# Kernel tuning notes

Hardware: AMD Instinct MI355X
Metric: run time of the kernel (lower is better)

## Reference

```python
import jax, jax.numpy as jnp
import numpy as np
from jax import lax

D_MODEL = 1024
EXPAND = 2
D_INNER = EXPAND * D_MODEL        # 2048
D_STATE = 16
D_CONV = 4
DT_RANK = (D_MODEL + 15) // 16    # 64, standard 'auto' dt_rank
BATCH, SEQ = 2, 1024


def setup_inputs() -> dict:
    key = jax.random.key(0)
    ks = jax.random.split(key, 10)
    g = lambda k, shape, sc: jax.random.normal(k, shape, jnp.float32) * sc
    A_log = jnp.log(jnp.broadcast_to(
        jnp.arange(1, D_STATE + 1, dtype=jnp.float32), (D_INNER, D_STATE)))
    return {
        "x": jax.random.normal(ks[0], (BATCH, SEQ, D_MODEL), jnp.float32),
        "gamma": jnp.ones((D_MODEL,), jnp.float32),
        "beta": jnp.zeros((D_MODEL,), jnp.float32),
        "W_in": g(ks[1], (D_MODEL, 2 * D_INNER), 0.02),
        "W_conv": g(ks[2], (D_INNER, D_CONV), 0.1),
        "b_conv": jnp.zeros((D_INNER,), jnp.float32),
        "W_x": g(ks[3], (D_INNER, DT_RANK + 2 * D_STATE), 0.02),
        "W_dt": g(ks[4], (DT_RANK, D_INNER), 0.1),
        "b_dt": g(ks[5], (D_INNER,), 0.1),
        "A_log": A_log,
        "Dskip": jnp.ones((D_INNER,), jnp.float32),
        "W_out": g(ks[6], (D_INNER, D_MODEL), 0.02),
    }


def _layernorm(x, gamma, beta, eps=1e-5):
    mu = jnp.mean(x, axis=-1, keepdims=True)
    var = jnp.mean(jnp.square(x - mu), axis=-1, keepdims=True)
    return (x - mu) * lax.rsqrt(var + eps) * gamma + beta


def _mamba_block(x, gamma, beta, W_in, W_conv, b_conv, W_x, W_dt, b_dt,
                 A_log, Dskip, W_out):
    h = _layernorm(x, gamma, beta)                       # [B,L,D]
    xz = h @ W_in                                        # [B,L,2*Din]
    xi, z = jnp.split(xz, 2, axis=-1)                    # each [B,L,Din]

    # depthwise causal conv over time
    xt = xi.transpose(0, 2, 1)                           # [B,Din,L]
    conv = lax.conv_general_dilated(
        xt, W_conv[:, None, :], window_strides=(1,),
        padding=[(D_CONV - 1, 0)], feature_group_count=D_INNER)
    u = jax.nn.silu(conv + b_conv[None, :, None]).transpose(0, 2, 1)  # [B,L,Din]

    x_dbl = u @ W_x                                      # [B,L,dt_rank+2N]
    dt_r = x_dbl[..., :DT_RANK]
    Bm = x_dbl[..., DT_RANK:DT_RANK + D_STATE]           # [B,L,N]
    Cm = x_dbl[..., DT_RANK + D_STATE:]                  # [B,L,N]
    dt = jax.nn.softplus(dt_r @ W_dt + b_dt)             # [B,L,Din]

    A = -jnp.exp(A_log)                                  # [Din,N]

    def step(hstate, inp):
        dt_s, B_s, C_s, u_s = inp                        # [B,Din],[B,N],[B,N],[B,Din]
        dA = jnp.exp(dt_s[..., None] * A)                # [B,Din,N]
        hstate = dA * hstate + (dt_s * u_s)[..., None] * B_s[:, None, :]
        y = jnp.einsum('bdn,bn->bd', hstate, C_s)
        return hstate, y

    h0 = jnp.zeros((x.shape[0], D_INNER, D_STATE), x.dtype)
    _, ys = lax.scan(step, h0, (dt.transpose(1, 0, 2), Bm.transpose(1, 0, 2),
                                Cm.transpose(1, 0, 2), u.transpose(1, 0, 2)))
    y = ys.transpose(1, 0, 2) + u * Dskip                # [B,L,Din]
    y = y * jax.nn.silu(z)
    return x + y @ W_out                                 # residual


def reference(x, gamma, beta, W_in, W_conv, b_conv, W_x, W_dt, b_dt,
              A_log, Dskip, W_out):
    return _mamba_block(x, gamma, beta, W_in, W_conv, b_conv, W_x, W_dt,
                        b_dt, A_log, Dskip, W_out)
```

## Files before the change

### kernel.cpp

```cpp
#include <hip/hip_runtime.h>
#include <math.h>

#define BB 2
#define SS 1024
#define DM 1024
#define DI 2048
#define DSTATE 16
#define DTR 64
#define NX 96
#define ROWS (BB*SS)
#define NCHUNK 16
#define LC (SS/NCHUNK)
#define NCH (BB*DI)
#define TS 16
#define NT (LC/TS)
#define KSPLIT 4
#define KSX 16

typedef __bf16 bf16x8 __attribute__((ext_vector_type(8)));
typedef float f32x4 __attribute__((ext_vector_type(4)));

static __device__ __forceinline__ unsigned short f2bf(float f) {
    unsigned u = __builtin_bit_cast(unsigned, f);
    unsigned r = (u + 0x7fff + ((u >> 16) & 1)) >> 16;
    return (unsigned short)r;
}
static __device__ __forceinline__ float bf2f(unsigned short v) {
    return __builtin_bit_cast(float, ((unsigned)v) << 16);
}

__device__ __forceinline__ void transpose_body(const float* __restrict__ W,
                                               unsigned short* __restrict__ WT,
                                               int K, int N, int bx, int by,
                                               unsigned short (*tile)[33]) {
    int n0 = bx * 32, k0 = by * 32;
    int tx = threadIdx.x & 31, ty = threadIdx.x >> 5;
#pragma unroll
    for (int r = 0; r < 4; r++)
        tile[ty + r * 8][tx] = f2bf(W[(size_t)(k0 + ty + r * 8) * N + n0 + tx]);
    __syncthreads();
#pragma unroll
    for (int r = 0; r < 4; r++)
        WT[(size_t)(n0 + ty + r * 8) * K + k0 + tx] = tile[tx][ty + r * 8];
}

__global__ __launch_bounds__(256) void prep_kernel(const float* __restrict__ x,
                                                   const float* __restrict__ gamma,
                                                   const float* __restrict__ beta,
                                                   unsigned short* __restrict__ h,
                                                   const float* __restrict__ W_in,
                                                   unsigned short* __restrict__ W_inT,
                                                   const float* __restrict__ W_out,
                                                   unsigned short* __restrict__ W_outT,
                                                   const float* __restrict__ W_x,
                                                   unsigned short* __restrict__ W_xT,
                                                   const float* __restrict__ W_dt,
                                                   unsigned short* __restrict__ W_dtT) {
    __shared__ unsigned short tile[32][33];
    __shared__ float red[4], red2[4];
    int blk = blockIdx.x;
    if (blk < ROWS) {
        int row = blk;
        const float* xr = x + (size_t)row * DM;
        float v[4];
        float s = 0.f;
#pragma unroll
        for (int i = 0; i < 4; i++) { v[i] = xr[threadIdx.x + i * 256]; s += v[i]; }
        int lane = threadIdx.x & 63, wid = threadIdx.x >> 6;
#pragma unroll
        for (int m = 1; m < 64; m <<= 1) s += __shfl_xor(s, m);
        if (lane == 0) red[wid] = s;
        __syncthreads();
        float mean = (red[0] + red[1] + red[2] + red[3]) * (1.0f / DM);
        float vs = 0.f;
#pragma unroll
        for (int i = 0; i < 4; i++) { float dv = v[i] - mean; vs += dv * dv; }
#pragma unroll
        for (int m = 1; m < 64; m <<= 1) vs += __shfl_xor(vs, m);
        if (lane == 0) red2[wid] = vs;
        __syncthreads();
        float var = (red2[0] + red2[1] + red2[2] + red2[3]) * (1.0f / DM);
        float inv = rsqrtf(var + 1e-5f);
        unsigned short* hr = h + (size_t)row * DM;
#pragma unroll
        for (int i = 0; i < 4; i++) {
            int idx = threadIdx.x + i * 256;
            hr[idx] = f2bf((v[i] - mean) * inv * gamma[idx] + beta[idx]);
        }
        return;
    }
    blk -= ROWS;
    if (blk < 4096) { transpose_body(W_in, W_inT, DM, 2 * DI, blk % 128, blk / 128, tile); return; }
    blk -= 4096;
    if (blk < 2048) { transpose_body(W_out, W_outT, DI, DM, blk % 32, blk / 32, tile); return; }
    blk -= 2048;
    if (blk < 192) { transpose_body(W_x, W_xT, DI, NX, blk % 3, blk / 3, tile); return; }
    blk -= 192;
    transpose_body(W_dt, W_dtT, DTR, DI, blk % 64, blk / 64, tile);
}

__global__ __launch_bounds__(256) void gemm_mfma_bfout(const __bf16* __restrict__ A,
                                                       const __bf16* __restrict__ BT,
                                                       unsigned short* __restrict__ C,
                                                       int M, int N, int K) {
    __shared__ __bf16 As[128 * 32];
    __shared__ __bf16 Bs[128 * 32];
    int tid = threadIdx.x;
    int w = tid >> 6, lane = tid & 63;
    int wr = w >> 1, wc = w & 1;
    int m0 = blockIdx.y * 128, n0 = blockIdx.x * 128;
    f32x4 acc[4][4] = {};
    int srow = lane >> 2, sgran = lane & 3;
    const __bf16* gA = A + (size_t)(m0 + w * 32) * K;
    const __bf16* gB = BT + (size_t)(n0 + w * 32) * K;
    int fr = lane & 15, q = lane >> 4;

    for (int k0 = 0; k0 < K; k0 += 32) {
        __syncthreads();
#pragma unroll
        for (int c = 0; c < 2; c++) {
            const __bf16* ga = gA + (size_t)(c * 16 + srow) * K + k0 + sgran * 8;
            const __bf16* gb = gB + (size_t)(c * 16 + srow) * K + k0 + sgran * 8;
            __builtin_amdgcn_global_load_lds(
                (const __attribute__((address_space(1))) void*)ga,
                (__attribute__((address_space(3))) void*)&As[(w * 32 + c * 16) * 32], 16, 0, 0);
            __builtin_amdgcn_global_load_lds(
                (const __attribute__((address_space(1))) void*)gb,
                (__attribute__((address_space(3))) void*)&Bs[(w * 32 + c * 16) * 32], 16, 0, 0);
        }
        __syncthreads();
        bf16x8 af[4], bfr[4];
#pragma unroll
        for (int i = 0; i < 4; i++)
            af[i] = *(const bf16x8*)&As[(wr * 64 + i * 16 + fr) * 32 + q * 8];
#pragma unroll
        for (int j = 0; j < 4; j++)
            bfr[j] = *(const bf16x8*)&Bs[(wc * 64 + j * 16 + fr) * 32 + q * 8];
#pragma unroll
        for (int i = 0; i < 4; i++)
#pragma unroll
            for (int j = 0; j < 4; j++)
                acc[i][j] = __builtin_amdgcn_mfma_f32_16x16x32_bf16(af[i], bfr[j], acc[i][j], 0, 0, 0);
    }
#pragma unroll
    for (int i = 0; i < 4; i++)
#pragma unroll
        for (int j = 0; j < 4; j++)
#pragma unroll
            for (int r = 0; r < 4; r++) {
                size_t ro = (size_t)(m0 + wr * 64 + i * 16 + q * 4 + r) * N
                          + n0 + wc * 64 + j * 16 + fr;
                C[ro] = f2bf(acc[i][j][r]);
            }
}

__global__ __launch_bounds__(256) void gemm_mfma_splitk(const __bf16* __restrict__ A,
                                                        const __bf16* __restrict__ BT,
                                                        unsigned short* __restrict__ part,
                                                        int M, int N, int K) {
    __shared__ __bf16 As[128 * 32];
    __shared__ __bf16 Bs[128 * 32];
    int tid = threadIdx.x;
    int w = tid >> 6, lane = tid & 63;
    int wr = w >> 1, wc = w & 1;
    int m0 = blockIdx.y * 128, n0 = blockIdx.x * 128;
    int ks = K / KSPLIT;
    int kbase = blockIdx.z * ks;
    f32x4 acc[4][4] = {};
    int srow = lane >> 2, sgran = lane & 3;
    const __bf16* gA = A + (size_t)(m0 + w * 32) * K + kbase;
    const __bf16* gB = BT + (size_t)(n0 + w * 32) * K + kbase;
    int fr = lane & 15, q = lane >> 4;

    for (int k0 = 0; k0 < ks; k0 += 32) {
        __syncthreads();
#pragma unroll
        for (int c = 0; c < 2; c++) {
            const __bf16* ga = gA + (size_t)(c * 16 + srow) * K + k0 + sgran * 8;
            const __bf16* gb = gB + (size_t)(c * 16 + srow) * K + k0 + sgran * 8;
            __builtin_amdgcn_global_load_lds(
                (const __attribute__((address_space(1))) void*)ga,
                (__attribute__((address_space(3))) void*)&As[(w * 32 + c * 16) * 32], 16, 0, 0);
            __builtin_amdgcn_global_load_lds(
                (const __attribute__((address_space(1))) void*)gb,
                (__attribute__((address_space(3))) void*)&Bs[(w * 32 + c * 16) * 32], 16, 0, 0);
        }
        __syncthreads();
        bf16x8 af[4], bfr[4];
#pragma unroll
        for (int i = 0; i < 4; i++)
            af[i] = *(const bf16x8*)&As[(wr * 64 + i * 16 + fr) * 32 + q * 8];
#pragma unroll
        for (int j = 0; j < 4; j++)
            bfr[j] = *(const bf16x8*)&Bs[(wc * 64 + j * 16 + fr) * 32 + q * 8];
#pragma unroll
        for (int i = 0; i < 4; i++)
#pragma unroll
            for (int j = 0; j < 4; j++)
                acc[i][j] = __builtin_amdgcn_mfma_f32_16x16x32_bf16(af[i], bfr[j], acc[i][j], 0, 0, 0);
    }
    unsigned short* Cp = part + (size_t)blockIdx.z * M * N;
#pragma unroll
    for (int i = 0; i < 4; i++)
#pragma unroll
        for (int j = 0; j < 4; j++)
#pragma unroll
            for (int r = 0; r < 4; r++) {
                size_t ro = (size_t)(m0 + wr * 64 + i * 16 + q * 4 + r) * N
                          + n0 + wc * 64 + j * 16 + fr;
                Cp[ro] = f2bf(acc[i][j][r]);
            }
}

__global__ __launch_bounds__(256) void reduce_splitk(const unsigned short* __restrict__ part,
                                                     const float* __restrict__ x,
                                                     float* __restrict__ out) {
    size_t i4 = ((size_t)blockIdx.x * 256 + threadIdx.x) * 4;
    const size_t slice = (size_t)ROWS * DM;
    f32x4 s = *(const f32x4*)(x + i4);
#pragma unroll
    for (int z = 0; z < KSPLIT; z++) {
        ushort4 p = *(const ushort4*)(part + z * slice + i4);
        s.x += bf2f(p.x); s.y += bf2f(p.y); s.z += bf2f(p.z); s.w += bf2f(p.w);
    }
    *(f32x4*)(out + i4) = s;
}

__global__ __launch_bounds__(256) void gemm_mfma_xdbl(const __bf16* __restrict__ A,
                                                      const __bf16* __restrict__ BT,
                                                      unsigned short* __restrict__ part_x) {
    __shared__ __bf16 As[128 * 32];
    __shared__ __bf16 Bs[128 * 32];
    int tid = threadIdx.x;
    int w = tid >> 6, lane = tid & 63;
    int wr = w >> 1, wc = w & 1;
    int m0 = blockIdx.y * 128;
    int srow = lane >> 2, sgran = lane & 3;
    int fr = lane & 15, q = lane >> 4;
    f32x4 acc[4][4] = {};
    const int ks = DI / KSX;
    const int kbase = blockIdx.z * ks;
    const __bf16* gA = A + (size_t)(m0 + w * 32) * DI + kbase;

    for (int k0 = 0; k0 < ks; k0 += 32) {
        __syncthreads();
#pragma unroll
        for (int c = 0; c < 2; c++) {
            const __bf16* ga = gA + (size_t)(c * 16 + srow) * DI + k0 + sgran * 8;
            int brow = w * 32 + c * 16 + srow;
            if (brow > 95) brow = 95;
            const __bf16* gb = BT + (size_t)brow * DI + kbase + k0 + sgran * 8;
            __builtin_amdgcn_global_load_lds(
                (const __attribute__((address_space(1))) void*)ga,
                (__attribute__((address_space(3))) void*)&As[(w * 32 + c * 16) * 32], 16, 0, 0);
            __builtin_amdgcn_global_load_lds(
                (const __attribute__((address_space(1))) void*)gb,
                (__attribute__((address_space(3))) void*)&Bs[(w * 32 + c * 16) * 32], 16, 0, 0);
        }
        __syncthreads();
        bf16x8 af[4], bfr[4];
#pragma unroll
        for (int i = 0; i < 4; i++)
            af[i] = *(const bf16x8*)&As[(wr * 64 + i * 16 + fr) * 32 + q * 8];
#pragma unroll
        for (int j = 0; j < 4; j++)
            bfr[j] = *(const bf16x8*)&Bs[(wc * 64 + j * 16 + fr) * 32 + q * 8];
#pragma unroll
        for (int i = 0; i < 4; i++)
#pragma unroll
            for (int j = 0; j < 4; j++)
                acc[i][j] = __builtin_amdgcn_mfma_f32_16x16x32_bf16(af[i], bfr[j], acc[i][j], 0, 0, 0);
    }
    unsigned short* Cp = part_x + (size_t)blockIdx.z * ROWS * NX;
#pragma unroll
    for (int i = 0; i < 4; i++)
#pragma unroll
        for (int j = 0; j < 4; j++) {
            int col = wc * 64 + j * 16 + fr;
            if (col < NX) {
#pragma unroll
                for (int r = 0; r < 4; r++) {
                    int row = m0 + wr * 64 + i * 16 + q * 4 + r;
                    Cp[(size_t)row * NX + col] = f2bf(acc[i][j][r]);
                }
            }
        }
}

__global__ __launch_bounds__(256) void reduce_xdbl(const unsigned short* __restrict__ part_x,
                                                   float* __restrict__ xdbl,
                                                   unsigned short* __restrict__ dtr_bf) {
    int idx = blockIdx.x * 256 + threadIdx.x;
    const size_t slice = (size_t)ROWS * NX;
    float s = 0.f;
#pragma unroll
    for (int z = 0; z < KSX; z++) s += bf2f(part_x[z * slice + idx]);
    xdbl[idx] = s;
    int col = idx % NX;
    if (col < DTR) {
        int row = idx / NX;
        dtr_bf[(size_t)row * DTR + col] = f2bf(s);
    }
}

__global__ __launch_bounds__(256) void dt_gemm(const __bf16* __restrict__ A,
                                               const __bf16* __restrict__ BT,
                                               const float* __restrict__ b_dt,
                                               unsigned short* __restrict__ dt) {
    __shared__ __bf16 As[128 * 32];
    __shared__ __bf16 Bs[128 * 32];
    int tid = threadIdx.x;
    int w = tid >> 6, lane = tid & 63;
    int wr = w >> 1, wc = w & 1;
    int m0 = blockIdx.y * 128, n0 = blockIdx.x * 128;
    int srow = lane >> 2, sgran = lane & 3;
    int fr = lane & 15, q = lane >> 4;
    f32x4 acc[4][4] = {};
    const __bf16* gA = A + (size_t)(m0 + w * 32) * DTR;
    const __bf16* gB = BT + (size_t)(n0 + w * 32) * DTR;

    for (int k0 = 0; k0 < DTR; k0 += 32) {
        __syncthreads();
#pragma unroll
        for (int c = 0; c < 2; c++) {
            const __bf16* ga = gA + (size_t)(c * 16 + srow) * DTR + k0 + sgran * 8;
            const __bf16* gb = gB + (size_t)(c * 16 + srow) * DTR + k0 + sgran * 8;
            __builtin_amdgcn_global_load_lds(
                (const __attribute__((address_space(1))) void*)ga,
                (__attribute__((address_space(3))) void*)&As[(w * 32 + c * 16) * 32], 16, 0, 0);
            __builtin_amdgcn_global_load_lds(
                (const __attribute__((address_space(1))) void*)gb,
                (__attribute__((address_space(3))) void*)&Bs[(w * 32 + c * 16) * 32], 16, 0, 0);
        }
        __syncthreads();
        bf16x8 af[4], bfr[4];
#pragma unroll
        for (int i = 0; i < 4; i++)
            af[i] = *(const bf16x8*)&As[(wr * 64 + i * 16 + fr) * 32 + q * 8];
#pragma unroll
        for (int j = 0; j < 4; j++)
            bfr[j] = *(const bf16x8*)&Bs[(wc * 64 + j * 16 + fr) * 32 + q * 8];
#pragma unroll
        for (int i = 0; i < 4; i++)
#pragma unroll
            for (int j = 0; j < 4; j++)
                acc[i][j] = __builtin_amdgcn_mfma_f32_16x16x32_bf16(af[i], bfr[j], acc[i][j], 0, 0, 0);
    }
#pragma unroll
    for (int i = 0; i < 4; i++)
#pragma unroll
        for (int j = 0; j < 4; j++) {
            int col = n0 + wc * 64 + j * 16 + fr;
            float bv = b_dt[col];
#pragma unroll
            for (int r = 0; r < 4; r++) {
                int row = m0 + wr * 64 + i * 16 + q * 4 + r;
                float a = acc[i][j][r] + bv;
                float sp = (a > 20.f) ? a : log1pf(expf(a));
                dt[(size_t)row * DI + col] = f2bf(sp);
            }
        }
}

__global__ __launch_bounds__(256) void conv_silu(const __bf16* __restrict__ xz,
                                                 const float* __restrict__ Wc,
                                                 const float* __restrict__ bc,
                                                 unsigned short* __restrict__ u_bf) {
    int idx = blockIdx.x * 256 + threadIdx.x;
    int d = idx & (DI - 1);
    int row = idx >> 11;
    int tpos = row & (SS - 1);
    float acc = bc[d];
#pragma unroll
    for (int k = 0; k < 4; k++) {
        int tt = tpos - 3 + k;
        if (tt >= 0) acc += (float)xz[(size_t)(row - 3 + k) * (2 * DI) + d] * Wc[d * 4 + k];
    }
    float s = acc / (1.f + __expf(-acc));
    u_bf[idx] = f2bf(s);
}

__global__ __launch_bounds__(256) void scan_chunk1(const __bf16* __restrict__ dt,
                                                   const __bf16* __restrict__ u,
                                                   const float* __restrict__ xdbl,
                                                   const float* __restrict__ A_log,
                                                   float* __restrict__ Aprod,
                                                   float* __restrict__ hloc) {
    __shared__ __bf16 dts[TS * 256];
    __shared__ __bf16 us_[TS * 256];
    __shared__ float bs[LC * DSTATE];
    int tid = threadIdx.x;
    int d0 = blockIdx.x * 256;
    int db = d0 & (DI - 1);
    int j = blockIdx.y;
    int c = d0 + tid;
    int b = c >> 11;
    int d = c & (DI - 1);
    int w = tid >> 6, lane = tid & 63;
    int halfrow = lane >> 5;
    int cw = (lane & 31) * 8;
    size_t r0 = (size_t)b * SS + (size_t)j * LC;

    {
        int row = tid >> 2, col = (tid & 3) * 4;
        f32x4 v = *(const f32x4*)(xdbl + (r0 + row) * NX + DTR + col);
        *(f32x4*)&bs[row * DSTATE + col] = v;
    }
    float Av[DSTATE], h[DSTATE], P[DSTATE];
#pragma unroll
    for (int q = 0; q < 4; q++) {
        f32x4 al = *(const f32x4*)(A_log + (size_t)d * DSTATE + q * 4);
#pragma unroll
        for (int e = 0; e < 4; e++) {
            Av[q * 4 + e] = -expf(al[e]);
            h[q * 4 + e] = 0.f;
            P[q * 4 + e] = 1.f;
        }
    }

    for (int tile = 0; tile < NT; tile++) {
        int t0 = tile * TS;
#pragma unroll
        for (int i = 0; i < 2; i++) {
            int rl = w * 4 + i * 2;
            const __bf16* gdt = dt + (size_t)(r0 + t0 + rl + halfrow) * DI + db + cw;
            const __bf16* gu  = u  + (size_t)(r0 + t0 + rl + halfrow) * DI + db + cw;
            __builtin_amdgcn_global_load_lds(
                (const __attribute__((address_space(1))) void*)gdt,
                (__attribute__((address_space(3))) void*)&dts[rl * 256], 16, 0, 0);
            __builtin_amdgcn_global_load_lds(
                (const __attribute__((address_space(1))) void*)gu,
                (__attribute__((address_space(3))) void*)&us_[rl * 256], 16, 0, 0);
        }
        __syncthreads();
#pragma unroll
        for (int t = 0; t < TS; t++) {
            float dtv = (float)dts[t * 256 + tid];
            float uv  = (float)us_[t * 256 + tid];
            float du = dtv * uv;
            const float* br = &bs[(t0 + t) * DSTATE];
            f32x4 Bq[4] = {*(const f32x4*)&br[0], *(const f32x4*)&br[4],
                           *(const f32x4*)&br[8], *(const f32x4*)&br[12]};
#pragma unroll
            for (int n = 0; n < DSTATE; n++) {
                float dA = __expf(dtv * Av[n]);
                P[n] *= dA;
                h[n] = dA * h[n] + du * Bq[n >> 2][n & 3];
            }
        }
        __syncthreads();
    }
    f32x4* Po = (f32x4*)(Aprod + ((size_t)j * NCH + c) * DSTATE);
    f32x4* ho = (f32x4*)(hloc + ((size_t)j * NCH + c) * DSTATE);
#pragma unroll
    for (int q = 0; q < 4; q++) {
        Po[q] = *(f32x4*)&P[q * 4];
        ho[q] = *(f32x4*)&h[q * 4];
    }
}

__global__ __launch_bounds__(256) void scan_chunk2(const __bf16* __restrict__ dt,
                                                   const __bf16* __restrict__ u,
                                                   const float* __restrict__ xdbl,
                                                   const float* __restrict__ A_log,
                                                   const float* __restrict__ Aprod,
                                                   const float* __restrict__ hloc,
                                                   const __bf16* __restrict__ xz,
                                                   const float* __restrict__ Dskip,
                                                   unsigned short* __restrict__ y2) {
    __shared__ __bf16 dts[TS * 256];
    __shared__ __bf16 us_[TS * 256];
    __shared__ __bf16 zs[TS * 256];
    __shared__ float bcs[LC * 2 * DSTATE];
    int tid = threadIdx.x;
    int d0 = blockIdx.x * 256;
    int db = d0 & (DI - 1);
    int j = blockIdx.y;
    int c = d0 + tid;
    int b = c >> 11;
    int d = c & (DI - 1);
    int w = tid >> 6, lane = tid & 63;
    int halfrow = lane >> 5;
    int cw = (lane & 31) * 8;
    size_t r0 = (size_t)b * SS + (size_t)j * LC;

    {
        int row = tid >> 2, col = (tid & 3) * 8;
        const float* src = xdbl + (r0 + row) * NX + DTR + col;
        f32x4 v0 = *(const f32x4*)src;
        f32x4 v1 = *(const f32x4*)(src + 4);
        *(f32x4*)&bcs[row * 32 + col] = v0;
        *(f32x4*)&bcs[row * 32 + col + 4] = v1;
    }
    float Av[DSTATE], h[DSTATE];
#pragma unroll
    for (int q = 0; q < 4; q++) {
        f32x4 al = *(const f32x4*)(A_log + (size_t)d * DSTATE + q * 4);
#pragma unroll
        for (int e = 0; e < 4; e++) {
            Av[q * 4 + e] = -expf(al[e]);
            h[q * 4 + e] = 0.f;
        }
    }
    for (int jj = 0; jj < j; jj++) {
        const f32x4* Pp = (const f32x4*)(Aprod + ((size_t)jj * NCH + c) * DSTATE);
        const f32x4* Hp = (const f32x4*)(hloc + ((size_t)jj * NCH + c) * DSTATE);
#pragma unroll
        for (int q = 0; q < 4; q++) {
            f32x4 P = Pp[q], H = Hp[q];
#pragma unroll
            for (int e = 0; e < 4; e++)
                h[q * 4 + e] = P[e] * h[q * 4 + e] + H[e];
        }
    }
    float Dv = Dskip[d];

    for (int tile = 0; tile < NT; tile++) {
        int t0 = tile * TS;
#pragma unroll
        for (int i = 0; i < 2; i++) {
            int rl = w * 4 + i * 2;
            const __bf16* gdt = dt + (size_t)(r0 + t0 + rl + halfrow) * DI + db + cw;
            const __bf16* gu  = u  + (size_t)(r0 + t0 + rl + halfrow) * DI + db + cw;
            const __bf16* gz  = xz + (size_t)(r0 + t0 + rl + halfrow) * (2 * DI) + DI + db + cw;
            __builtin_amdgcn_global_load_lds(
                (const __attribute__((address_space(1))) void*)gdt,
                (__attribute__((address_space(3))) void*)&dts[rl * 256], 16, 0, 0);
            __builtin_amdgcn_global_load_lds(
                (const __attribute__((address_space(1))) void*)gu,
                (__attribute__((address_space(3))) void*)&us_[rl * 256], 16, 0, 0);
            __builtin_amdgcn_global_load_lds(
                (const __attribute__((address_space(1))) void*)gz,
                (__attribute__((address_space(3))) void*)&zs[rl * 256], 16, 0, 0);
        }
        __syncthreads();
#pragma unroll
        for (int t = 0; t < TS; t++) {
            float dtv = (float)dts[t * 256 + tid];
            float uv  = (float)us_[t * 256 + tid];
            float zz  = (float)zs[t * 256 + tid];
            float du = dtv * uv;
            const float* br = &bcs[(t0 + t) * 32];
            f32x4 Bq[4] = {*(const f32x4*)&br[0], *(const f32x4*)&br[4],
                           *(const f32x4*)&br[8], *(const f32x4*)&br[12]};
            f32x4 Cq[4] = {*(const f32x4*)&br[16], *(const f32x4*)&br[20],
                           *(const f32x4*)&br[24], *(const f32x4*)&br[28]};
            float p = 0.f;
#pragma unroll
            for (int n = 0; n < DSTATE; n++) {
                float dA = __expf(dtv * Av[n]);
                h[n] = dA * h[n] + du * Bq[n >> 2][n & 3];
                p += h[n] * Cq[n >> 2][n & 3];
            }
            float sz = zz / (1.f + __expf(-zz));
            y2[(r0 + t0 + t) * DI + d] = f2bf((p + uv * Dv) * sz);
        }
        __syncthreads();
    }
}

extern "C" void kernel_launch(void* const* d_in, const int* in_sizes, int n_in,
                              void* d_out, int out_size, void* d_ws, size_t ws_size,
                              hipStream_t stream) {
    const float* x      = (const float*)d_in[0];
    const float* gamma  = (const float*)d_in[1];
    const float* beta   = (const float*)d_in[2];
    const float* W_in   = (const float*)d_in[3];
    const float* W_conv = (const float*)d_in[4];
    const float* b_conv = (const float*)d_in[5];
    const float* W_x    = (const float*)d_in[6];
    const float* W_dt   = (const float*)d_in[7];
    const float* b_dt   = (const float*)d_in[8];
    const float* A_log  = (const float*)d_in[9];
    const float* Dskip  = (const float*)d_in[10];
    const float* W_out  = (const float*)d_in[11];
    float* out = (float*)d_out;

    float* ws     = (float*)d_ws;
    float* xdbl   = ws;
    float* Aprod  = xdbl + (size_t)ROWS * NX;
    float* hloc   = Aprod + (size_t)NCHUNK * NCH * DSTATE;
    unsigned short* part   = (unsigned short*)(hloc + (size_t)NCHUNK * NCH * DSTATE);
    unsigned short* part_x = part + (size_t)KSPLIT * ROWS * DM;
    unsigned short* xz_bf  = part_x + (size_t)KSX * ROWS * NX;
    unsigned short* u_bf   = xz_bf + (size_t)ROWS * 2 * DI;
    unsigned short* dt_bf  = u_bf + (size_t)ROWS * DI;
    unsigned short* h_bf   = dt_bf + (size_t)ROWS * DI;
    unsigned short* y_bf   = h_bf + (size_t)ROWS * DM;
    unsigned short* W_inT  = y_bf + (size_t)ROWS * DI;
    unsigned short* W_outT = W_inT + (size_t)(2 * DI) * DM;
    unsigned short* W_xT   = W_outT + (size_t)DM * DI;
    unsigned short* W_dtT  = W_xT + (size_t)NX * DI;
    unsigned short* dtr_bf = W_dtT + (size_t)DI * DTR;

    prep_kernel<<<ROWS + 4096 + 2048 + 192 + 128, 256, 0, stream>>>(
        x, gamma, beta, h_bf, W_in, W_inT, W_out, W_outT, W_x, W_xT, W_dt, W_dtT);
    gemm_mfma_bfout<<<dim3(2 * DI / 128, ROWS / 128), 256, 0, stream>>>(
        (const __bf16*)h_bf, (const __bf16*)W_inT, xz_bf, ROWS, 2 * DI, DM);
    conv_silu<<<ROWS * DI / 256, 256, 0, stream>>>((const __bf16*)xz_bf, W_conv, b_conv, u_bf);
    gemm_mfma_xdbl<<<dim3(1, ROWS / 128, KSX), 256, 0, stream>>>(
        (const __bf16*)u_bf, (const __bf16*)W_xT, part_x);
    reduce_xdbl<<<(ROWS * NX) / 256, 256, 0, stream>>>(part_x, xdbl, dtr_bf);
    dt_gemm<<<dim3(DI / 128, ROWS / 128), 256, 0, stream>>>(
        (const __bf16*)dtr_bf, (const __bf16*)W_dtT, b_dt, dt_bf);
    scan_chunk1<<<dim3(NCH / 256, NCHUNK), 256, 0, stream>>>(
        (const __bf16*)dt_bf, (const __bf16*)u_bf, xdbl, A_log, Aprod, hloc);
    scan_chunk2<<<dim3(NCH / 256, NCHUNK), 256, 0, stream>>>(
        (const __bf16*)dt_bf, (const __bf16*)u_bf, xdbl, A_log, Aprod, hloc,
        (const __bf16*)xz_bf, Dskip, y_bf);
    gemm_mfma_splitk<<<dim3(DM / 128, ROWS / 128, KSPLIT), 256, 0, stream>>>(
        (const __bf16*)y_bf, (const __bf16*)W_outT, part, ROWS, DM, DI);
    reduce_splitk<<<(ROWS * DM) / (256 * 4), 256, 0, stream>>>(part, x, out);
}
```

Measured before the change: 272.3 us.

## Fuse split-K x_dbl reduction into dt GEMM and scan kernels; double scan chunks

Removes the separate reduce_xdbl kernel and its fp32 xdbl buffer. dt_gemm now sums the KSX bf16 partials for its 128-row tile into LDS, and the scan kernels sum the B/C partials directly when loading them. NCHUNK also goes from 16 to 32, which doubles scan parallelism but makes the sequential prefix loop in scan_chunk2 longer. The cost is redundant reduction work: each dt_gemm column block and each scan channel block re-reads all 16 partial slices, so more global reads replace one launch.

```diff
diff --git a/kernel.cpp b/kernel.cpp
--- a/kernel.cpp
+++ b/kernel.cpp
@@ -9,7 +9,7 @@
 #define DTR 64
 #define NX 96
 #define ROWS (BB*SS)
-#define NCHUNK 16
+#define NCHUNK 32
 #define LC (SS/NCHUNK)
 #define NCH (BB*DI)
 #define TS 16
@@ -287,27 +287,11 @@
         }
 }
 
-__global__ __launch_bounds__(256) void reduce_xdbl(const unsigned short* __restrict__ part_x,
-                                                   float* __restrict__ xdbl,
-                                                   unsigned short* __restrict__ dtr_bf) {
-    int idx = blockIdx.x * 256 + threadIdx.x;
-    const size_t slice = (size_t)ROWS * NX;
-    float s = 0.f;
-#pragma unroll
-    for (int z = 0; z < KSX; z++) s += bf2f(part_x[z * slice + idx]);
-    xdbl[idx] = s;
-    int col = idx % NX;
-    if (col < DTR) {
-        int row = idx / NX;
-        dtr_bf[(size_t)row * DTR + col] = f2bf(s);
-    }
-}
-
-__global__ __launch_bounds__(256) void dt_gemm(const __bf16* __restrict__ A,
+__global__ __launch_bounds__(256) void dt_gemm(const unsigned short* __restrict__ part_x,
                                                const __bf16* __restrict__ BT,
                                                const float* __restrict__ b_dt,
                                                unsigned short* __restrict__ dt) {
-    __shared__ __bf16 As[128 * 32];
+    __shared__ __bf16 As[128 * 72];
     __shared__ __bf16 Bs[128 * 32];
     int tid = threadIdx.x;
     int w = tid >> 6, lane = tid & 63;
@@ -316,18 +300,35 @@
     int srow = lane >> 2, sgran = lane & 3;
     int fr = lane & 15, q = lane >> 4;
     f32x4 acc[4][4] = {};
-    const __bf16* gA = A + (size_t)(m0 + w * 32) * DTR;
+    const size_t slice = (size_t)ROWS * NX;
     const __bf16* gB = BT + (size_t)(n0 + w * 32) * DTR;
 
+    {
+        int lrow = tid >> 1;
+        int c0 = (tid & 1) * 32;
+        float accv[32];
+#pragma unroll
+        for (int e = 0; e < 32; e++) accv[e] = 0.f;
+        const unsigned short* base = part_x + (size_t)(m0 + lrow) * NX + c0;
+        for (int z = 0; z < KSX; z++) {
+            const __bf16* src = (const __bf16*)(base + z * slice);
+#pragma unroll
+            for (int v = 0; v < 4; v++) {
+                bf16x8 pv = *(const bf16x8*)(src + v * 8);
+#pragma unroll
+                for (int e = 0; e < 8; e++) accv[v * 8 + e] += (float)pv[e];
+            }
+        }
+        unsigned short* dst = (unsigned short*)&As[lrow * 72 + c0];
+#pragma unroll
+        for (int e = 0; e < 32; e++) dst[e] = f2bf(accv[e]);
+    }
+
     for (int k0 = 0; k0 < DTR; k0 += 32) {
         __syncthreads();
 #pragma unroll
         for (int c = 0; c < 2; c++) {
-            const __bf16* ga = gA + (size_t)(c * 16 + srow) * DTR + k0 + sgran * 8;
             const __bf16* gb = gB + (size_t)(c * 16 + srow) * DTR + k0 + sgran * 8;
-            __builtin_amdgcn_global_load_lds(
-                (const __attribute__((address_space(1))) void*)ga,
-                (__attribute__((address_space(3))) void*)&As[(w * 32 + c * 16) * 32], 16, 0, 0);
             __builtin_amdgcn_global_load_lds(
                 (const __attribute__((address_space(1))) void*)gb,
                 (__attribute__((address_space(3))) void*)&Bs[(w * 32 + c * 16) * 32], 16, 0, 0);
@@ -336,7 +337,7 @@
         bf16x8 af[4], bfr[4];
 #pragma unroll
         for (int i = 0; i < 4; i++)
-            af[i] = *(const bf16x8*)&As[(wr * 64 + i * 16 + fr) * 32 + q * 8];
+            af[i] = *(const bf16x8*)&As[(wr * 64 + i * 16 + fr) * 72 + k0 + q * 8];
 #pragma unroll
         for (int j = 0; j < 4; j++)
             bfr[j] = *(const bf16x8*)&Bs[(wc * 64 + j * 16 + fr) * 32 + q * 8];
@@ -382,7 +383,7 @@
 
 __global__ __launch_bounds__(256) void scan_chunk1(const __bf16* __restrict__ dt,
                                                    const __bf16* __restrict__ u,
-                                                   const float* __restrict__ xdbl,
+                                                   const unsigned short* __restrict__ part_x,
                                                    const float* __restrict__ A_log,
                                                    float* __restrict__ Aprod,
                                                    float* __restrict__ hloc) {
@@ -400,11 +401,18 @@
     int halfrow = lane >> 5;
     int cw = (lane & 31) * 8;
     size_t r0 = (size_t)b * SS + (size_t)j * LC;
+    const size_t slice = (size_t)ROWS * NX;
 
     {
-        int row = tid >> 2, col = (tid & 3) * 4;
-        f32x4 v = *(const f32x4*)(xdbl + (r0 + row) * NX + DTR + col);
-        *(f32x4*)&bs[row * DSTATE + col] = v;
+#pragma unroll
+        for (int ee = 0; ee < 2; ee++) {
+            int e = tid * 2 + ee;
+            int row = e >> 4, n = e & 15;
+            const unsigned short* src = part_x + (r0 + row) * NX + DTR + n;
+            float s = 0.f;
+            for (int z = 0; z < KSX; z++) s += bf2f(src[z * slice]);
+            bs[row * DSTATE + n] = s;
+        }
     }
     float Av[DSTATE], h[DSTATE], P[DSTATE];
 #pragma unroll
@@ -461,7 +469,7 @@
 
 __global__ __launch_bounds__(256) void scan_chunk2(const __bf16* __restrict__ dt,
                                                    const __bf16* __restrict__ u,
-                                                   const float* __restrict__ xdbl,
+                                                   const unsigned short* __restrict__ part_x,
                                                    const float* __restrict__ A_log,
                                                    const float* __restrict__ Aprod,
                                                    const float* __restrict__ hloc,
@@ -483,14 +491,18 @@
     int halfrow = lane >> 5;
     int cw = (lane & 31) * 8;
     size_t r0 = (size_t)b * SS + (size_t)j * LC;
+    const size_t slice = (size_t)ROWS * NX;
 
     {
-        int row = tid >> 2, col = (tid & 3) * 8;
-        const float* src = xdbl + (r0 + row) * NX + DTR + col;
-        f32x4 v0 = *(const f32x4*)src;
-        f32x4 v1 = *(const f32x4*)(src + 4);
-        *(f32x4*)&bcs[row * 32 + col] = v0;
-        *(f32x4*)&bcs[row * 32 + col + 4] = v1;
+#pragma unroll
+        for (int ee = 0; ee < 4; ee++) {
+            int e = tid * 4 + ee;
+            int row = e >> 5, n = e & 31;
+            const unsigned short* src = part_x + (r0 + row) * NX + DTR + n;
+            float s = 0.f;
+            for (int z = 0; z < KSX; z++) s += bf2f(src[z * slice]);
+            bcs[row * 32 + n] = s;
+        }
     }
     float Av[DSTATE], h[DSTATE];
 #pragma unroll
@@ -577,8 +589,7 @@
     float* out = (float*)d_out;
 
     float* ws     = (float*)d_ws;
-    float* xdbl   = ws;
-    float* Aprod  = xdbl + (size_t)ROWS * NX;
+    float* Aprod  = ws;
     float* hloc   = Aprod + (size_t)NCHUNK * NCH * DSTATE;
     unsigned short* part   = (unsigned short*)(hloc + (size_t)NCHUNK * NCH * DSTATE);
     unsigned short* part_x = part + (size_t)KSPLIT * ROWS * DM;
@@ -591,7 +602,6 @@
     unsigned short* W_outT = W_inT + (size_t)(2 * DI) * DM;
     unsigned short* W_xT   = W_outT + (size_t)DM * DI;
     unsigned short* W_dtT  = W_xT + (size_t)NX * DI;
-    unsigned short* dtr_bf = W_dtT + (size_t)DI * DTR;
 
     prep_kernel<<<ROWS + 4096 + 2048 + 192 + 128, 256, 0, stream>>>(
         x, gamma, beta, h_bf, W_in, W_inT, W_out, W_outT, W_x, W_xT, W_dt, W_dtT);
@@ -600,13 +610,12 @@
     conv_silu<<<ROWS * DI / 256, 256, 0, stream>>>((const __bf16*)xz_bf, W_conv, b_conv, u_bf);
     gemm_mfma_xdbl<<<dim3(1, ROWS / 128, KSX), 256, 0, stream>>>(
         (const __bf16*)u_bf, (const __bf16*)W_xT, part_x);
-    reduce_xdbl<<<(ROWS * NX) / 256, 256, 0, stream>>>(part_x, xdbl, dtr_bf);
     dt_gemm<<<dim3(DI / 128, ROWS / 128), 256, 0, stream>>>(
-        (const __bf16*)dtr_bf, (const __bf16*)W_dtT, b_dt, dt_bf);
+        part_x, (const __bf16*)W_dtT, b_dt, dt_bf);
     scan_chunk1<<<dim3(NCH / 256, NCHUNK), 256, 0, stream>>>(
-        (const __bf16*)dt_bf, (const __bf16*)u_bf, xdbl, A_log, Aprod, hloc);
+        (const __bf16*)dt_bf, (const __bf16*)u_bf, part_x, A_log, Aprod, hloc);
     scan_chunk2<<<dim3(NCH / 256, NCHUNK), 256, 0, stream>>>(
-        (const __bf16*)dt_bf, (const __bf16*)u_bf, xdbl, A_log, Aprod, hloc,
+        (const __bf16*)dt_bf, (const __bf16*)u_bf, part_x, A_log, Aprod, hloc,
         (const __bf16*)xz_bf, Dskip, y_bf);
     gemm_mfma_splitk<<<dim3(DM / 128, ROWS / 128, KSPLIT), 256, 0, stream>>>(
         (const __bf16*)y_bf, (const __bf16*)W_outT, part, ROWS, DM, DI);
```

New measurement: 289.4 us. +6.3%, slower.
